# Performance work log

Hardware: AMD Instinct MI355X
Metric: run time of the kernel (lower is better)

## Reference

```python
import jax, jax.numpy as jnp
import numpy as np

B, N, T, DIN, DOUT, H = 8, 512, 128, 128, 128, 8
HD = DOUT // H  # head_dim


def setup_inputs() -> dict:
    key = jax.random.key(0)
    ks = jax.random.split(key, 9)
    h = jax.random.normal(ks[0], (B, N, T, DIN), dtype=jnp.float32)
    adj = jax.random.uniform(ks[1], (B, T, N, 1), dtype=jnp.float32)
    mask = jax.random.randint(ks[2], (B, N, T, 1), 0, 2).astype(jnp.float32)
    s1 = 1.0 / np.sqrt(DIN)
    W1 = jax.random.uniform(ks[3], (DIN, DOUT), jnp.float32, -s1, s1)
    b1 = jax.random.uniform(ks[4], (DOUT,), jnp.float32, -s1, s1)
    sa = 1.0 / np.sqrt(2 * HD)
    Wa = jax.random.uniform(ks[5], (2 * HD, 1), jnp.float32, -sa, sa)
    ba = jax.random.uniform(ks[6], (1,), jnp.float32, -sa, sa)
    s2 = 1.0 / np.sqrt(2 * DOUT)
    W2 = jax.random.uniform(ks[7], (2 * DOUT, DOUT), jnp.float32, -s2, s2)
    b2 = jax.random.uniform(ks[8], (DOUT,), jnp.float32, -s2, s2)
    return {"h": h, "adj": adj, "mask": mask, "W1": W1, "b1": b1,
            "Wa": Wa, "ba": ba, "W2": W2, "b2": b2}


def reference(h, adj, mask, W1, b1, Wa, ba, W2, b2):
    # h: (B,N,T,DIN) -> project to (B,N,T,DOUT)
    hp = jnp.einsum('bntd,de->bnte', h, W1) + b1
    target_h = hp[:, 0]                      # (B,T,DOUT)
    # (B,T,H,N,HD)
    hh = hp.reshape(B, N, T, H, HD).transpose(0, 2, 3, 1, 4)
    # Original builds an NxNx2HD concat then a Linear and keeps only src-row 0.
    # Equivalent additive decomposition: score = h0.Wsrc + hj.Wdst + b.
    Wsrc, Wdst = Wa[:HD, 0], Wa[HD:, 0]
    s0 = jnp.einsum('bthd,d->bth', hh[:, :, :, 0], Wsrc)   # (B,T,H)
    sj = jnp.einsum('bthnd,d->bthn', hh, Wdst)             # (B,T,H,N)
    score = s0[..., None] + sj + ba[0]                     # (B,T,H,N)
    # mask: (B,N,T,1) -> (B,T,1,N), broadcast over heads
    m = mask[:, :, :, 0].transpose(0, 2, 1)[:, :, None, :]
    # adj: (B,T,N,1) -> (B,T,1,N)
    a = adj[:, :, :, 0][:, :, None, :]
    a = jnp.where(a == 0, 1e9, a)
    a = jnp.where(m > 0, 1.0 / a, a)
    score = jnp.where(m == 0, -1e9, score)
    attn = jax.nn.softmax(score, axis=-1) * a              # (B,T,H,N)
    agg = jnp.einsum('bthn,bthnd->bthd', attn, hh).reshape(B, T, DOUT)
    out = jnp.concatenate([agg, target_h], axis=-1) @ W2 + b2
    return out
```

## Files before the change

### kernel.cpp

```cpp
#include <hip/hip_runtime.h>

#define NN   512
#define TT   128
#define DD   128
#define NC   64
#define NCHUNK 8
#define SR   132
#define WR   68

__global__ void gat_prep(const float* __restrict__ W1, const float* __restrict__ b1,
                         const float* __restrict__ Wa, const float* __restrict__ ba,
                         float* __restrict__ ws)
{
  int idx = blockIdx.x*256 + threadIdx.x;
  int d = idx >> 3, h = idx & 7;
  float v = 0.f, u = 0.f;
  for (int j = 0; j < 16; ++j){
    float w1 = W1[d*DD + h*16 + j];
    v += w1 * Wa[16 + j];
    u += w1 * Wa[j];
  }
  ws[(h>>1)*256 + (d>>2)*8 + (h&1)*4 + (d&3)] = v;
  ws[2048 + d*8 + h] = u;
  if (idx < 8){
    float ec = ba[0];
    for (int j = 0; j < 16; ++j)
      ec += b1[idx*16 + j] * (Wa[j] + Wa[16 + j]);
    ws[3072 + idx] = ec;
  }
}

__global__ __launch_bounds__(256, 4) void gat_main(
    const float* __restrict__ hin, const float* __restrict__ adj, const float* __restrict__ mask,
    const float* __restrict__ W1,  const float* __restrict__ b1,
    const float* __restrict__ W2,  const float* __restrict__ b2,
    const float* __restrict__ ws,  float* __restrict__ out)
{
  __shared__ __align__(16) float hchd[NC*SR];
  __shared__ __align__(16) float vsh[1024];
  __shared__ __align__(16) float wTt[8*WR];
  __shared__ float scaleS[8], ZL[8], SWL[8], Karr[8];
  __shared__ float targ[128];

  float* const aggfin = hchd;
  float* const catbuf = hchd + 8*SR;
  float* const oppart = hchd + 8*SR + 256;

  const int t    = threadIdx.x;
  const int bb   = blockIdx.x >> 7;
  const int tt   = blockIdx.x & 127;
  const int wave = t >> 6;
  const int lane = t & 63;

  #pragma unroll
  for (int r = 0; r < 4; ++r) vsh[t + 256*r] = ws[t + 256*r];

  float mrun0 = -1e30f, mrun1 = -1e30f;
  float Z0 = 0.f, Z1 = 0.f, SW0 = 0.f, SW1 = 0.f;
  float acc0 = 0.f, acc1 = 0.f, acc2 = 0.f, acc3 = 0.f;

  const int dq = t & 31;
  const int hh = t >> 5;

  const float4* __restrict__ hg4 = (const float4*)hin;
  const long g0 = ((long)(bb*NN + (t>>5))*TT + tt)*(DD/4) + (t & 31);
  const int  l0 = (t>>5)*SR + 4*(t & 31);

  for (int c = 0; c < NCHUNK; ++c){
    {
      const long gc = g0 + (long)c * (NC*TT*(DD/4));
      #pragma unroll
      for (int i = 0; i < 8; ++i)
        *(float4*)&hchd[l0 + i*(8*SR)] = hg4[gc + (long)i*(8*TT*(DD/4))];
    }
    __syncthreads();

    if (c == 0){
      if (t < 128){
        float a = b1[t];
        for (int d = 0; d < 128; ++d)
          a += hchd[d] * W1[d*DD + t];
        targ[t] = a;
      } else if (t < 136){
        int h8 = t - 128;
        float a = ws[3072 + h8];
        for (int d = 0; d < 128; ++d)
          a += hchd[d] * ws[2048 + d*8 + h8];
        Karr[h8] = a;
      }
      __syncthreads();
    }

    float s0 = Karr[2*wave], s1 = Karr[2*wave + 1];
    {
      const float4* rowp = (const float4*)&hchd[lane*SR];
      const float4* vp   = (const float4*)&vsh[wave*256];
      #pragma unroll 8
      for (int j = 0; j < 32; ++j){
        float4 r4 = rowp[j];
        float4 va = vp[2*j], vb = vp[2*j + 1];
        s0 += r4.x*va.x + r4.y*va.y + r4.z*va.z + r4.w*va.w;
        s1 += r4.x*vb.x + r4.y*vb.y + r4.z*vb.z + r4.w*vb.w;
      }
    }
    const int ng = c*NC + lane;
    const float mv   = mask[(long)(bb*NN + ng)*TT + tt];
    const float av   = adj[(long)(bb*TT + tt)*NN + ng];
    const float inva = (av == 0.f) ? 1e-9f : (1.f/av);

    float sm0 = (mv > 0.f) ? s0 : -1e30f;
    float sm1 = (mv > 0.f) ? s1 : -1e30f;
    #pragma unroll
    for (int off = 32; off >= 1; off >>= 1){
      sm0 = fmaxf(sm0, __shfl_xor(sm0, off));
      sm1 = fmaxf(sm1, __shfl_xor(sm1, off));
    }
    float mn0 = fmaxf(mrun0, sm0), mn1 = fmaxf(mrun1, sm1);
    float sc0 = __expf(mrun0 - mn0), sc1 = __expf(mrun1 - mn1);
    mrun0 = mn0; mrun1 = mn1;

    float e0 = (mv > 0.f) ? __expf(s0 - mn0) : 0.f;
    float e1 = (mv > 0.f) ? __expf(s1 - mn1) : 0.f;
    float w0 = e0*inva, w1 = e1*inva;
    wTt[(2*wave)*WR + lane]     = w0;
    wTt[(2*wave + 1)*WR + lane] = w1;
    if (lane == 0){ scaleS[2*wave] = sc0; scaleS[2*wave + 1] = sc1; }

    float z0 = e0, z1 = e1, y0 = w0, y1 = w1;
    #pragma unroll
    for (int off = 32; off >= 1; off >>= 1){
      z0 += __shfl_xor(z0, off); z1 += __shfl_xor(z1, off);
      y0 += __shfl_xor(y0, off); y1 += __shfl_xor(y1, off);
    }
    Z0 = Z0*sc0 + z0;   Z1 = Z1*sc1 + z1;
    SW0 = SW0*sc0 + y0; SW1 = SW1*sc1 + y1;
    __syncthreads();

    {
      float scl = scaleS[hh];
      acc0 *= scl; acc1 *= scl; acc2 *= scl; acc3 *= scl;
      #pragma unroll 4
      for (int nb = 0; nb < 16; ++nb){
        float4 w4 = *(const float4*)&wTt[hh*WR + 4*nb];
        float4 r0 = *(const float4*)&hchd[(4*nb + 0)*SR + 4*dq];
        float4 r1 = *(const float4*)&hchd[(4*nb + 1)*SR + 4*dq];
        float4 r2 = *(const float4*)&hchd[(4*nb + 2)*SR + 4*dq];
        float4 r3 = *(const float4*)&hchd[(4*nb + 3)*SR + 4*dq];
        acc0 += w4.x*r0.x + w4.y*r1.x + w4.z*r2.x + w4.w*r3.x;
        acc1 += w4.x*r0.y + w4.y*r1.y + w4.z*r2.y + w4.w*r3.y;
        acc2 += w4.x*r0.z + w4.y*r1.z + w4.z*r2.z + w4.w*r3.z;
        acc3 += w4.x*r0.w + w4.y*r1.w + w4.z*r2.w + w4.w*r3.w;
      }
    }
    __syncthreads();
  }

  if (lane == 0){
    ZL[2*wave] = Z0;  ZL[2*wave + 1] = Z1;
    SWL[2*wave] = SW0; SWL[2*wave + 1] = SW1;
  }
  __syncthreads();
  {
    float invZ = 1.f / ZL[hh];
    float4 o; o.x = acc0*invZ; o.y = acc1*invZ; o.z = acc2*invZ; o.w = acc3*invZ;
    *(float4*)&aggfin[hh*SR + 4*dq] = o;
  }
  __syncthreads();

  if (t < 128){
    int h2 = t >> 4;
    float a = (SWL[h2] / ZL[h2]) * b1[t];
    for (int d = 0; d < 128; ++d)
      a += aggfin[h2*SR + d] * W1[d*DD + t];
    catbuf[t]       = a;
    catbuf[128 + t] = targ[t];
  }
  __syncthreads();

  {
    int j = t & 127, kh = t >> 7;
    float o = 0.f;
    for (int k = kh*128; k < kh*128 + 128; ++k)
      o += catbuf[k] * W2[k*DD + j];
    oppart[t] = o;
  }
  __syncthreads();
  if (t < 128)
    out[(long)blockIdx.x*128 + t] = oppart[t] + oppart[128 + t] + b2[t];
}

extern "C" void kernel_launch(void* const* d_in, const int* in_sizes, int n_in,
                              void* d_out, int out_size, void* d_ws, size_t ws_size,
                              hipStream_t stream) {
  const float* h    = (const float*)d_in[0];
  const float* adj  = (const float*)d_in[1];
  const float* mask = (const float*)d_in[2];
  const float* W1   = (const float*)d_in[3];
  const float* b1   = (const float*)d_in[4];
  const float* Wa   = (const float*)d_in[5];
  const float* ba   = (const float*)d_in[6];
  const float* W2   = (const float*)d_in[7];
  const float* b2   = (const float*)d_in[8];
  float* ws  = (float*)d_ws;
  float* out = (float*)d_out;

  gat_prep<<<4, 256, 0, stream>>>(W1, b1, Wa, ba, ws);
  gat_main<<<1024, 256, 0, stream>>>(h, adj, mask, W1, b1, W2, b2, ws, out);
}
```

Measured before the change: 416.7 us.

## Prefetch next h chunk into registers and make per-wave aggregation self-contained

Each iteration now loads the next 64-row chunk of h into registers while computing scores and aggregation on the current one, then writes it to LDS after a barrier, so global latency overlaps compute. The aggregation is remapped so each wave handles its own two heads, with lanes splitting rows in two halves and combining them with a shuffle at the end. This removes the shared scale array and one barrier per chunk. Softmax sums become per-lane partials reduced once after the loop, and the Wa-projected vectors are read from global/L1 instead of staged in LDS. The cost is more registers (8 float4 prefetch plus 8 accumulators), which may reduce occupancy under launch_bounds(256,4).

```diff
diff --git a/kernel.cpp b/kernel.cpp
--- a/kernel.cpp
+++ b/kernel.cpp
@@ -37,9 +37,8 @@
     const float* __restrict__ ws,  float* __restrict__ out)
 {
   __shared__ __align__(16) float hchd[NC*SR];
-  __shared__ __align__(16) float vsh[1024];
   __shared__ __align__(16) float wTt[8*WR];
-  __shared__ float scaleS[8], ZL[8], SWL[8], Karr[8];
+  __shared__ float Karr[8], RL[8];
   __shared__ float targ[128];
 
   float* const aggfin = hchd;
@@ -51,61 +50,70 @@
   const int tt   = blockIdx.x & 127;
   const int wave = t >> 6;
   const int lane = t & 63;
-
-  #pragma unroll
-  for (int r = 0; r < 4; ++r) vsh[t + 256*r] = ws[t + 256*r];
+  const int h0   = 2*wave;
+
+  const int wv = __builtin_amdgcn_readfirstlane(wave);
+  const float4* __restrict__ vg = (const float4*)(ws + (wv << 8));
+
+  const int dq = lane & 31;
+  const int rh = lane >> 5;
 
   float mrun0 = -1e30f, mrun1 = -1e30f;
-  float Z0 = 0.f, Z1 = 0.f, SW0 = 0.f, SW1 = 0.f;
+  float Zp0 = 0.f, Zp1 = 0.f, SWp0 = 0.f, SWp1 = 0.f;
   float acc0 = 0.f, acc1 = 0.f, acc2 = 0.f, acc3 = 0.f;
-
-  const int dq = t & 31;
-  const int hh = t >> 5;
+  float acc4 = 0.f, acc5 = 0.f, acc6 = 0.f, acc7 = 0.f;
 
   const float4* __restrict__ hg4 = (const float4*)hin;
+  const long dI = 8L*TT*(DD/4);
+  const long dC = (long)NC*TT*(DD/4);
   const long g0 = ((long)(bb*NN + (t>>5))*TT + tt)*(DD/4) + (t & 31);
   const int  l0 = (t>>5)*SR + 4*(t & 31);
 
+  float4 pf[8];
+  #pragma unroll
+  for (int i = 0; i < 8; ++i) pf[i] = hg4[g0 + (long)i*dI];
+  #pragma unroll
+  for (int i = 0; i < 8; ++i) *(float4*)&hchd[l0 + i*(8*SR)] = pf[i];
+  __syncthreads();
+
+  if (t < 128){
+    float a = b1[t];
+    for (int d = 0; d < 128; ++d)
+      a += hchd[d] * W1[d*DD + t];
+    targ[t] = a;
+  } else if (t < 136){
+    int h8 = t - 128;
+    float a = ws[3072 + h8];
+    for (int d = 0; d < 128; ++d)
+      a += hchd[d] * ws[2048 + d*8 + h8];
+    Karr[h8] = a;
+  }
+  __syncthreads();
+
+  const float K0 = Karr[h0], K1 = Karr[h0 + 1];
+
   for (int c = 0; c < NCHUNK; ++c){
-    {
-      const long gc = g0 + (long)c * (NC*TT*(DD/4));
+    const int ng = c*NC + lane;
+    const float mv = mask[(long)(bb*NN + ng)*TT + tt];
+    const float av = adj[(long)(bb*TT + tt)*NN + ng];
+
+    if (c < NCHUNK-1){
+      const long gc = g0 + (long)(c+1)*dC;
       #pragma unroll
-      for (int i = 0; i < 8; ++i)
-        *(float4*)&hchd[l0 + i*(8*SR)] = hg4[gc + (long)i*(8*TT*(DD/4))];
-    }
-    __syncthreads();
-
-    if (c == 0){
-      if (t < 128){
-        float a = b1[t];
-        for (int d = 0; d < 128; ++d)
-          a += hchd[d] * W1[d*DD + t];
-        targ[t] = a;
-      } else if (t < 136){
-        int h8 = t - 128;
-        float a = ws[3072 + h8];
-        for (int d = 0; d < 128; ++d)
-          a += hchd[d] * ws[2048 + d*8 + h8];
-        Karr[h8] = a;
-      }
-      __syncthreads();
-    }
-
-    float s0 = Karr[2*wave], s1 = Karr[2*wave + 1];
+      for (int i = 0; i < 8; ++i) pf[i] = hg4[gc + (long)i*dI];
+    }
+
+    float s0 = K0, s1 = K1;
     {
       const float4* rowp = (const float4*)&hchd[lane*SR];
-      const float4* vp   = (const float4*)&vsh[wave*256];
       #pragma unroll 8
       for (int j = 0; j < 32; ++j){
         float4 r4 = rowp[j];
-        float4 va = vp[2*j], vb = vp[2*j + 1];
+        float4 va = vg[2*j], vb = vg[2*j + 1];
         s0 += r4.x*va.x + r4.y*va.y + r4.z*va.z + r4.w*va.w;
         s1 += r4.x*vb.x + r4.y*vb.y + r4.z*vb.z + r4.w*vb.w;
       }
     }
-    const int ng = c*NC + lane;
-    const float mv   = mask[(long)(bb*NN + ng)*TT + tt];
-    const float av   = adj[(long)(bb*TT + tt)*NN + ng];
     const float inva = (av == 0.f) ? 1e-9f : (1.f/av);
 
     float sm0 = (mv > 0.f) ? s0 : -1e30f;
@@ -122,54 +130,72 @@
     float e0 = (mv > 0.f) ? __expf(s0 - mn0) : 0.f;
     float e1 = (mv > 0.f) ? __expf(s1 - mn1) : 0.f;
     float w0 = e0*inva, w1 = e1*inva;
-    wTt[(2*wave)*WR + lane]     = w0;
-    wTt[(2*wave + 1)*WR + lane] = w1;
-    if (lane == 0){ scaleS[2*wave] = sc0; scaleS[2*wave + 1] = sc1; }
-
-    float z0 = e0, z1 = e1, y0 = w0, y1 = w1;
-    #pragma unroll
-    for (int off = 32; off >= 1; off >>= 1){
-      z0 += __shfl_xor(z0, off); z1 += __shfl_xor(z1, off);
-      y0 += __shfl_xor(y0, off); y1 += __shfl_xor(y1, off);
-    }
-    Z0 = Z0*sc0 + z0;   Z1 = Z1*sc1 + z1;
-    SW0 = SW0*sc0 + y0; SW1 = SW1*sc1 + y1;
+    wTt[h0*WR + lane]       = w0;
+    wTt[(h0 + 1)*WR + lane] = w1;
+    Zp0  = Zp0*sc0  + e0;  Zp1  = Zp1*sc1  + e1;
+    SWp0 = SWp0*sc0 + w0;  SWp1 = SWp1*sc1 + w1;
+
+    {
+      acc0 *= sc0; acc1 *= sc0; acc2 *= sc0; acc3 *= sc0;
+      acc4 *= sc1; acc5 *= sc1; acc6 *= sc1; acc7 *= sc1;
+      const int rbase = rh*32;
+      const float* wr0 = &wTt[h0*WR + rbase];
+      const float* wr1 = &wTt[(h0 + 1)*WR + rbase];
+      const float* hb  = &hchd[rbase*SR + 4*dq];
+      #pragma unroll 4
+      for (int g = 0; g < 8; ++g){
+        float4 wa = *(const float4*)&wr0[4*g];
+        float4 wb = *(const float4*)&wr1[4*g];
+        float4 r0 = *(const float4*)&hb[(4*g + 0)*SR];
+        float4 r1 = *(const float4*)&hb[(4*g + 1)*SR];
+        float4 r2 = *(const float4*)&hb[(4*g + 2)*SR];
+        float4 r3 = *(const float4*)&hb[(4*g + 3)*SR];
+        acc0 += wa.x*r0.x + wa.y*r1.x + wa.z*r2.x + wa.w*r3.x;
+        acc1 += wa.x*r0.y + wa.y*r1.y + wa.z*r2.y + wa.w*r3.y;
+        acc2 += wa.x*r0.z + wa.y*r1.z + wa.z*r2.z + wa.w*r3.z;
+        acc3 += wa.x*r0.w + wa.y*r1.w + wa.z*r2.w + wa.w*r3.w;
+        acc4 += wb.x*r0.x + wb.y*r1.x + wb.z*r2.x + wb.w*r3.x;
+        acc5 += wb.x*r0.y + wb.y*r1.y + wb.z*r2.y + wb.w*r3.y;
+        acc6 += wb.x*r0.z + wb.y*r1.z + wb.z*r2.z + wb.w*r3.z;
+        acc7 += wb.x*r0.w + wb.y*r1.w + wb.z*r2.w + wb.w*r3.w;
+      }
+    }
     __syncthreads();
-
-    {
-      float scl = scaleS[hh];
-      acc0 *= scl; acc1 *= scl; acc2 *= scl; acc3 *= scl;
-      #pragma unroll 4
-      for (int nb = 0; nb < 16; ++nb){
-        float4 w4 = *(const float4*)&wTt[hh*WR + 4*nb];
-        float4 r0 = *(const float4*)&hchd[(4*nb + 0)*SR + 4*dq];
-        float4 r1 = *(const float4*)&hchd[(4*nb + 1)*SR + 4*dq];
-        float4 r2 = *(const float4*)&hchd[(4*nb + 2)*SR + 4*dq];
-        float4 r3 = *(const float4*)&hchd[(4*nb + 3)*SR + 4*dq];
-        acc0 += w4.x*r0.x + w4.y*r1.x + w4.z*r2.x + w4.w*r3.x;
-        acc1 += w4.x*r0.y + w4.y*r1.y + w4.z*r2.y + w4.w*r3.y;
-        acc2 += w4.x*r0.z + w4.y*r1.z + w4.z*r2.z + w4.w*r3.z;
-        acc3 += w4.x*r0.w + w4.y*r1.w + w4.z*r2.w + w4.w*r3.w;
-      }
-    }
-    __syncthreads();
-  }
+    if (c < NCHUNK-1){
+      #pragma unroll
+      for (int i = 0; i < 8; ++i) *(float4*)&hchd[l0 + i*(8*SR)] = pf[i];
+      __syncthreads();
+    }
+  }
+
+  #pragma unroll
+  for (int off = 32; off >= 1; off >>= 1){
+    Zp0  += __shfl_xor(Zp0,  off);  Zp1  += __shfl_xor(Zp1,  off);
+    SWp0 += __shfl_xor(SWp0, off);  SWp1 += __shfl_xor(SWp1, off);
+  }
+  acc0 += __shfl_xor(acc0, 32); acc1 += __shfl_xor(acc1, 32);
+  acc2 += __shfl_xor(acc2, 32); acc3 += __shfl_xor(acc3, 32);
+  acc4 += __shfl_xor(acc4, 32); acc5 += __shfl_xor(acc5, 32);
+  acc6 += __shfl_xor(acc6, 32); acc7 += __shfl_xor(acc7, 32);
 
   if (lane == 0){
-    ZL[2*wave] = Z0;  ZL[2*wave + 1] = Z1;
-    SWL[2*wave] = SW0; SWL[2*wave + 1] = SW1;
-  }
-  __syncthreads();
+    RL[h0]     = SWp0 / Zp0;
+    RL[h0 + 1] = SWp1 / Zp1;
+  }
   {
-    float invZ = 1.f / ZL[hh];
-    float4 o; o.x = acc0*invZ; o.y = acc1*invZ; o.z = acc2*invZ; o.w = acc3*invZ;
-    *(float4*)&aggfin[hh*SR + 4*dq] = o;
+    float invZ = (rh == 0) ? (1.f/Zp0) : (1.f/Zp1);
+    float4 o;
+    o.x = ((rh == 0) ? acc0 : acc4) * invZ;
+    o.y = ((rh == 0) ? acc1 : acc5) * invZ;
+    o.z = ((rh == 0) ? acc2 : acc6) * invZ;
+    o.w = ((rh == 0) ? acc3 : acc7) * invZ;
+    *(float4*)&aggfin[(h0 + rh)*SR + 4*dq] = o;
   }
   __syncthreads();
 
   if (t < 128){
     int h2 = t >> 4;
-    float a = (SWL[h2] / ZL[h2]) * b1[t];
+    float a = RL[h2] * b1[t];
     for (int d = 0; d < 128; ++d)
       a += aggfin[h2*SR + d] * W1[d*DD + t];
     catbuf[t]       = a;
```

After: 434.6 us. 1.04x slower.
